# Performance work log

Measured on AMD Instinct MI355X. Metric: run time of the kernel, lower is better.

## Reference

```python
import jax, jax.numpy as jnp
import numpy as np

B, T, C, H, F = 4, 1024, 1024, 16, 4096
D = C // H

def _ln(x, g, b):
    m = x.mean(-1, keepdims=True)
    v = ((x - m) ** 2).mean(-1, keepdims=True)
    return (x - m) * jax.lax.rsqrt(v + 1e-5) * g + b

def setup_inputs() -> dict:
    key = jax.random.key(0)
    ks = jax.random.split(key, 9)
    p = lambda k, shape: jax.random.normal(k, shape, jnp.float32) * 0.02
    return dict(
        x=jax.random.normal(ks[0], (B, T, C), jnp.float32),
        context=jax.random.normal(ks[1], (B, T, C), jnp.float32),
        ln1_g=jnp.ones((C,), jnp.float32), ln1_b=jnp.zeros((C,), jnp.float32),
        qkv_w=p(ks[2], (C, 3 * C)), qkv_b=jnp.zeros((3 * C,), jnp.float32),
        attn_out_w=p(ks[3], (C, C)), attn_out_b=jnp.zeros((C,), jnp.float32),
        lnc_g=jnp.ones((C,), jnp.float32), lnc_b=jnp.zeros((C,), jnp.float32),
        q_w=p(ks[4], (C, C)), q_b=jnp.zeros((C,), jnp.float32),
        kv_w=p(ks[5], (C, 2 * C)), kv_b=jnp.zeros((2 * C,), jnp.float32),
        cross_out_w=p(ks[6], (C, C)), cross_out_b=jnp.zeros((C,), jnp.float32),
        ln2_g=jnp.ones((C,), jnp.float32), ln2_b=jnp.zeros((C,), jnp.float32),
        ffn_w1=p(ks[7], (C, F)), ffn_b1=jnp.zeros((F,), jnp.float32),
        ffn_w2=p(ks[8], (F, C)), ffn_b2=jnp.zeros((C,), jnp.float32),
    )

def reference(x, context, ln1_g, ln1_b, qkv_w, qkv_b, attn_out_w, attn_out_b,
              lnc_g, lnc_b, q_w, q_b, kv_w, kv_b, cross_out_w, cross_out_b,
              ln2_g, ln2_b, ffn_w1, ffn_b1, ffn_w2, ffn_b2):
    scale = 1.0 / np.sqrt(D)
    # --- causal self-attention ---
    h = _ln(x, ln1_g, ln1_b)
    qkv = (h @ qkv_w + qkv_b).reshape(B, T, 3, H, D)
    q, k, v = qkv[:, :, 0], qkv[:, :, 1], qkv[:, :, 2]  # [B,T,H,D]
    s = jnp.einsum('bqhd,bkhd->bhqk', q, k) * scale     # [B,H,T,T]
    causal = jnp.tril(jnp.ones((T, T), bool))
    s = jnp.where(causal, s, -jnp.inf)
    a = jax.nn.softmax(s, axis=-1)
    o = jnp.einsum('bhqk,bkhd->bqhd', a, v).reshape(B, T, C)
    x = x + o @ attn_out_w + attn_out_b
    # --- cross-attention (query=x, context=encoder) ---
    h = _ln(x, lnc_g, lnc_b)
    q = (h @ q_w + q_b).reshape(B, T, H, D)
    kv = (context @ kv_w + kv_b).reshape(B, T, 2, H, D)
    k, v = kv[:, :, 0], kv[:, :, 1]
    s = jnp.einsum('bqhd,bkhd->bhqk', q, k) * scale
    a = jax.nn.softmax(s, axis=-1)
    o = jnp.einsum('bhqk,bkhd->bqhd', a, v).reshape(B, T, C)
    x = x + o @ cross_out_w + cross_out_b
    # --- FFN (exact GELU as in torch default) ---
    h = _ln(x, ln2_g, ln2_b)
    h = jax.nn.gelu(h @ ffn_w1 + ffn_b1, approximate=False)
    return x + h @ ffn_w2 + ffn_b2
```

## Files before the change

### kernel.cpp

```cpp
#include <hip/hip_runtime.h>
#include <hip/hip_bf16.h>

#define BT 4096
#define TT 1024
#define HN 16

typedef __attribute__((ext_vector_type(8))) short bf16x8;
typedef __attribute__((ext_vector_type(4))) float f32x4;
typedef __attribute__((ext_vector_type(16))) float f32x16;

__device__ __forceinline__ unsigned short f2bf(float f) {
    unsigned u = __builtin_bit_cast(unsigned, f);
    unsigned r = (u + 0x7fffu + ((u >> 16) & 1u)) >> 16;
    return (unsigned short)r;
}

__device__ __forceinline__ unsigned pk2bf(float a, float b) {
    return (unsigned)f2bf(a) | ((unsigned)f2bf(b) << 16);
}

__device__ __forceinline__ void g2l16(const void* g, void* l) {
    __builtin_amdgcn_global_load_lds(
        (__attribute__((address_space(1))) void*)(g),
        (__attribute__((address_space(3))) void*)(l), 16, 0, 0);
}

__device__ __forceinline__ float gelu_f(float v) {
    float t = v * (0.7978845608f + 0.0356774081f * v * v);
    float e = __expf(2.f * t);
    float th = 1.f - 2.f / (e + 1.f);
    return 0.5f * v * (1.f + th);
}

struct TransJobs {
    const float* W[7];
    unsigned short* Wt[7];
    int K[7], N[7];
    int start[8];
};

__device__ __forceinline__
void ln_row(const float* __restrict__ xr, const float* __restrict__ g,
            const float* __restrict__ bta, unsigned short* __restrict__ outr,
            float* red)
{
    float4 v = ((const float4*)xr)[threadIdx.x];
    float s = v.x + v.y + v.z + v.w;
    float q = v.x*v.x + v.y*v.y + v.z*v.z + v.w*v.w;
#pragma unroll
    for (int m = 1; m < 64; m <<= 1) {
        s += __shfl_xor(s, m, 64);
        q += __shfl_xor(q, m, 64);
    }
    int wave = threadIdx.x >> 6;
    if ((threadIdx.x & 63) == 0) { red[wave] = s; red[4 + wave] = q; }
    __syncthreads();
    s = red[0] + red[1] + red[2] + red[3];
    q = red[4] + red[5] + red[6] + red[7];
    float mean = s * (1.f / 1024.f);
    float var  = q * (1.f / 1024.f) - mean * mean;
    float rstd = rsqrtf(var + 1e-5f);
    float4 gv = ((const float4*)g)[threadIdx.x];
    float4 bv = ((const float4*)bta)[threadIdx.x];
    uint2 o;
    o.x = pk2bf((v.x - mean) * rstd * gv.x + bv.x, (v.y - mean) * rstd * gv.y + bv.y);
    o.y = pk2bf((v.z - mean) * rstd * gv.z + bv.z, (v.w - mean) * rstd * gv.w + bv.w);
    ((uint2*)outr)[threadIdx.x] = o;
}

__global__ __launch_bounds__(256)
void prep_kernel(TransJobs J, const float* __restrict__ x,
                 const float* __restrict__ g, const float* __restrict__ bta,
                 unsigned short* __restrict__ outx,
                 const float* __restrict__ ctx, unsigned short* __restrict__ outc)
{
    __shared__ float tile[32][33];
    __shared__ float red[8];
    int bid = blockIdx.x;
    const int nT = J.start[7];
    if (bid < nT) {
        int j = 0;
#pragma unroll
        for (int t = 0; t < 7; ++t)
            if (bid >= J.start[t + 1]) j = t + 1;
        int t = bid - J.start[j];
        int K = J.K[j], N = J.N[j];
        int ntx = N >> 5;
        int n0 = (t % ntx) * 32, k0 = (t / ntx) * 32;
        const float* W = J.W[j];
        unsigned short* Wt = J.Wt[j];
        int tx = threadIdx.x & 31, ty = threadIdx.x >> 5;
#pragma unroll
        for (int i = ty; i < 32; i += 8)
            tile[i][tx] = W[(size_t)(k0 + i) * N + n0 + tx];
        __syncthreads();
#pragma unroll
        for (int i = ty; i < 32; i += 8)
            Wt[(size_t)(n0 + i) * K + k0 + tx] = f2bf(tile[tx][i]);
    } else if (bid < nT + BT) {
        int row = bid - nT;
        ln_row(x + (size_t)row * 1024, g, bta, outx + (size_t)row * 1024, red);
    } else {
        size_t i = (size_t)(bid - nT - BT) * 256 + threadIdx.x;
        float4 v = ((const float4*)ctx)[i];
        uint2 o;
        o.x = pk2bf(v.x, v.y);
        o.y = pk2bf(v.z, v.w);
        ((uint2*)outc)[i] = o;
    }
}

__global__ __launch_bounds__(256)
void ln_kernel(const float* __restrict__ x, const float* __restrict__ g,
               const float* __restrict__ bta, unsigned short* __restrict__ out)
{
    __shared__ float red[8];
    int row = blockIdx.x;
    ln_row(x + (size_t)row * 1024, g, bta, out + (size_t)row * 1024, red);
}

__global__ __launch_bounds__(256)
void transpose_v(const unsigned short* __restrict__ v, unsigned short* __restrict__ vt,
                 int stride)
{
    __shared__ unsigned short tile[32][33];
    int d0 = blockIdx.x * 32, t0 = blockIdx.y * 32, bh = blockIdx.z;
    int b = bh >> 4, h = bh & 15;
    int tx = threadIdx.x, ty = threadIdx.y;
#pragma unroll
    for (int i = ty; i < 32; i += 8)
        tile[i][tx] = v[((size_t)b * TT + t0 + i) * stride + h * 64 + d0 + tx];
    __syncthreads();
#pragma unroll
    for (int i = ty; i < 32; i += 8)
        vt[((size_t)bh * 64 + d0 + i) * TT + t0 + tx] = tile[tx][i];
}

template<int MODE>
__device__ __forceinline__
void gemm_core(unsigned short* lA, unsigned short* lB,
               const unsigned short* __restrict__ A,
               const unsigned short* __restrict__ Bt,
               const float* __restrict__ bias,
               const float* __restrict__ res,
               void* __restrict__ outp,
               int N, int K, int m0, int n0, int kbeg, int kend)
{
    const int tid = threadIdx.x;
    const int wave = tid >> 6, lane = tid & 63;
    const int l32 = lane & 31, half = lane >> 5;
    const int sw = l32 & 7;
    const int wN = (wave >> 1) * 64;
    const int wM = (wave & 1) * 64;

    f32x16 acc[2][2];
#pragma unroll
    for (int i = 0; i < 2; ++i)
#pragma unroll
        for (int j = 0; j < 2; ++j)
#pragma unroll
            for (int r = 0; r < 16; ++r) acc[i][j][r] = 0.f;

    for (int k0 = kbeg; k0 < kend; k0 += 64) {
        __syncthreads();
#pragma unroll
        for (int it = 0; it < 4; ++it) {
            int chunk = it * 256 + tid;
            int row = chunk >> 3, slot = chunk & 7;
            int kc = slot ^ (row & 7);
            g2l16(A  + (size_t)(m0 + row) * K + k0 + kc * 8, &lA[chunk * 8]);
            g2l16(Bt + (size_t)(n0 + row) * K + k0 + kc * 8, &lB[chunk * 8]);
        }
        __syncthreads();
#pragma unroll
        for (int ks = 0; ks < 4; ++ks) {
            const int gc = ks * 2 + half;
            const int sl = (gc ^ sw) * 8;
            bf16x8 af[2], bfr[2];
#pragma unroll
            for (int i = 0; i < 2; ++i)
                af[i] = *(const bf16x8*)&lB[(wN + i * 32 + l32) * 64 + sl];
#pragma unroll
            for (int j = 0; j < 2; ++j)
                bfr[j] = *(const bf16x8*)&lA[(wM + j * 32 + l32) * 64 + sl];
#pragma unroll
            for (int i = 0; i < 2; ++i)
#pragma unroll
                for (int j = 0; j < 2; ++j)
                    acc[i][j] = __builtin_amdgcn_mfma_f32_32x32x16_bf16(af[i], bfr[j], acc[i][j], 0, 0, 0);
        }
    }

#pragma unroll
    for (int i = 0; i < 2; ++i) {
#pragma unroll
        for (int g = 0; g < 4; ++g) {
            const int nb = n0 + wN + i * 32 + g * 8 + half * 4;
            float4 bs;
            if (MODE != 3) bs = *(const float4*)&bias[nb];
#pragma unroll
            for (int j = 0; j < 2; ++j) {
                const int m = m0 + wM + j * 32 + l32;
                const size_t idx = (size_t)m * N + nb;
                float v0 = acc[i][j][g * 4 + 0], v1 = acc[i][j][g * 4 + 1];
                float v2 = acc[i][j][g * 4 + 2], v3 = acc[i][j][g * 4 + 3];
                if (MODE != 3) { v0 += bs.x; v1 += bs.y; v2 += bs.z; v3 += bs.w; }
                if (MODE == 1) { v0 = gelu_f(v0); v1 = gelu_f(v1); v2 = gelu_f(v2); v3 = gelu_f(v3); }
                if (MODE == 2) {
                    float4 rr = *(const float4*)&res[idx];
                    float4 o; o.x = v0 + rr.x; o.y = v1 + rr.y; o.z = v2 + rr.z; o.w = v3 + rr.w;
                    *(float4*)((float*)outp + idx) = o;
                } else if (MODE == 3) {
                    float4 o; o.x = v0; o.y = v1; o.z = v2; o.w = v3;
                    *(float4*)((float*)outp + idx) = o;
                } else {
                    uint2 u;
                    u.x = pk2bf(v0, v1);
                    u.y = pk2bf(v2, v3);
                    *(uint2*)((unsigned short*)outp + idx) = u;
                }
            }
        }
    }
}

template<int MODE>
__global__ __launch_bounds__(256)
void gemm_bt(const unsigned short* __restrict__ A,
             const unsigned short* __restrict__ Bt,
             const float* __restrict__ bias,
             const float* __restrict__ res,
             void* __restrict__ outp,
             int M, int N, int K)
{
    __shared__ unsigned short lA[128 * 64];
    __shared__ unsigned short lB[128 * 64];
    gemm_core<MODE>(lA, lB, A, Bt, bias, res, outp, N, K,
                    blockIdx.y * 128, blockIdx.x * 128, 0, K);
}

__global__ __launch_bounds__(256)
void gemm_dual(const unsigned short* __restrict__ A1, const unsigned short* __restrict__ B1,
               const float* __restrict__ b1, unsigned short* __restrict__ o1p, int N1, int nbx1,
               const unsigned short* __restrict__ A2, const unsigned short* __restrict__ B2,
               const float* __restrict__ b2, unsigned short* __restrict__ o2p, int N2,
               int K)
{
    __shared__ unsigned short lA[128 * 64];
    __shared__ unsigned short lB[128 * 64];
    int bx = blockIdx.x;
    if (bx < nbx1)
        gemm_core<0>(lA, lB, A1, B1, b1, nullptr, o1p, N1, K,
                     blockIdx.y * 128, bx * 128, 0, K);
    else
        gemm_core<0>(lA, lB, A2, B2, b2, nullptr, o2p, N2, K,
                     blockIdx.y * 128, (bx - nbx1) * 128, 0, K);
}

__global__ __launch_bounds__(256)
void gemm_splitk(const unsigned short* __restrict__ A,
                 const unsigned short* __restrict__ Bt,
                 float* __restrict__ part,
                 int M, int N, int K, int kslice)
{
    __shared__ unsigned short lA[128 * 64];
    __shared__ unsigned short lB[128 * 64];
    int kz = blockIdx.z;
    gemm_core<3>(lA, lB, A, Bt, nullptr, nullptr,
                 part + (size_t)kz * M * N, N, K,
                 blockIdx.y * 128, blockIdx.x * 128,
                 kz * kslice, (kz + 1) * kslice);
}

__global__ __launch_bounds__(256)
void reduce2(const float* __restrict__ part, const float* __restrict__ bias,
             const float* __restrict__ res, float* __restrict__ out, int MN)
{
    int i = blockIdx.x * 256 + threadIdx.x;
    const float4* p = (const float4*)part;
    int q = MN >> 2;
    float4 a = p[i], b = p[i + q];
    float4 bs = ((const float4*)bias)[i & 255];
    float4 rr = ((const float4*)res)[i];
    float4 o;
    o.x = a.x + b.x + bs.x + rr.x;
    o.y = a.y + b.y + bs.y + rr.y;
    o.z = a.z + b.z + bs.z + rr.z;
    o.w = a.w + b.w + bs.w + rr.w;
    ((float4*)out)[i] = o;
}

__global__ __launch_bounds__(256)
void gemm_small2(const unsigned short* __restrict__ A,
                 const unsigned short* __restrict__ Bt,
                 const float* __restrict__ bias,
                 const float* __restrict__ res,
                 float* __restrict__ outp,
                 int M, int N, int K)
{
    __shared__ unsigned short lA[64 * 64];
    __shared__ unsigned short lB[128 * 64];
    const int tid = threadIdx.x;
    const int wave = tid >> 6, lane = tid & 63;
    const int l32 = lane & 31, half = lane >> 5;
    const int sw = l32 & 7;
    const int m0 = blockIdx.y * 64, n0 = blockIdx.x * 128;
    const int wM = (wave >> 1) * 32;
    const int wN = (wave & 1) * 64;

    f32x16 acc[2];
#pragma unroll
    for (int i = 0; i < 2; ++i)
#pragma unroll
        for (int r = 0; r < 16; ++r) acc[i][r] = 0.f;

    for (int k0 = 0; k0 < K; k0 += 64) {
        __syncthreads();
#pragma unroll
        for (int it = 0; it < 6; ++it) {
            int chunk = it * 256 + tid;
            if (chunk < 512) {
                int row = chunk >> 3, slot = chunk & 7;
                int kc = slot ^ (row & 7);
                g2l16(A + (size_t)(m0 + row) * K + k0 + kc * 8, &lA[chunk * 8]);
            } else {
                int cb = chunk - 512;
                int row = cb >> 3, slot = cb & 7;
                int kc = slot ^ (row & 7);
                g2l16(Bt + (size_t)(n0 + row) * K + k0 + kc * 8, &lB[cb * 8]);
            }
        }
        __syncthreads();
#pragma unroll
        for (int ks = 0; ks < 4; ++ks) {
            const int gc = ks * 2 + half;
            const int sl = (gc ^ sw) * 8;
            bf16x8 bfr = *(const bf16x8*)&lA[(wM + l32) * 64 + sl];
            bf16x8 af[2];
#pragma unroll
            for (int i = 0; i < 2; ++i)
                af[i] = *(const bf16x8*)&lB[(wN + i * 32 + l32) * 64 + sl];
#pragma unroll
            for (int i = 0; i < 2; ++i)
                acc[i] = __builtin_amdgcn_mfma_f32_32x32x16_bf16(af[i], bfr, acc[i], 0, 0, 0);
        }
    }

#pragma unroll
    for (int i = 0; i < 2; ++i) {
#pragma unroll
        for (int g = 0; g < 4; ++g) {
            const int nb = n0 + wN + i * 32 + g * 8 + half * 4;
            float4 bs = *(const float4*)&bias[nb];
            const int m = m0 + wM + l32;
            const size_t idx = (size_t)m * N + nb;
            float4 rr = *(const float4*)&res[idx];
            float4 o;
            o.x = acc[i][g * 4 + 0] + bs.x + rr.x;
            o.y = acc[i][g * 4 + 1] + bs.y + rr.y;
            o.z = acc[i][g * 4 + 2] + bs.z + rr.z;
            o.w = acc[i][g * 4 + 3] + bs.w + rr.w;
            *(float4*)&outp[idx] = o;
        }
    }
}

__global__ __launch_bounds__(256)
void attn_kernel(const unsigned short* __restrict__ qp,
                 const unsigned short* __restrict__ kp,
                 const unsigned short* __restrict__ vt,
                 unsigned short* __restrict__ op,
                 int qstride, int kstride, int causal)
{
    __shared__ unsigned short lK[64 * 72];
    __shared__ unsigned short lV[64 * 72];
    __shared__ unsigned short lP[4][16 * 72];

    const int tid = threadIdx.x;
    const int wave = tid >> 6, lane = tid & 63;
    const int quad = lane >> 4, l16 = lane & 15;
    const int bh = blockIdx.y, b = bh >> 4, h = bh & 15;
    const int qtile = causal ? (gridDim.x - 1 - blockIdx.x) : blockIdx.x;
    const int q0 = qtile * 64;
    const size_t rowbase = (size_t)b * TT;
    const int hoff = h * 64;
    const unsigned short* vbase = vt + (size_t)bh * 64 * TT;

    bf16x8 qf[2];
    {
        int qrow = q0 + wave * 16 + l16;
        const unsigned short* qrp = qp + (rowbase + qrow) * (size_t)qstride + hoff;
        qf[0] = *(const bf16x8*)(qrp + quad * 8);
        qf[1] = *(const bf16x8*)(qrp + 32 + quad * 8);
    }

    f32x4 oacc[4];
#pragma unroll
    for (int jd = 0; jd < 4; ++jd)
#pragma unroll
        for (int r = 0; r < 4; ++r) oacc[jd][r] = 0.f;
    float mrun = -1e30f, lrun = 0.f;

    const int nkt = causal ? (qtile + 1) : (TT / 64);
    for (int kt = 0; kt < nkt; ++kt) {
        __syncthreads();
#pragma unroll
        for (int it = 0; it < 2; ++it) {
            int c = it * 256 + tid;
            int r8 = c >> 3, cc = c & 7;
            *(bf16x8*)&lK[r8 * 72 + cc * 8] =
                *(const bf16x8*)(kp + (rowbase + kt * 64 + r8) * (size_t)kstride + hoff + cc * 8);
            *(bf16x8*)&lV[r8 * 72 + cc * 8] =
                *(const bf16x8*)(vbase + (size_t)r8 * TT + kt * 64 + cc * 8);
        }
        __syncthreads();

        f32x4 s[4];
#pragma unroll
        for (int i = 0; i < 4; ++i)
#pragma unroll
            for (int r = 0; r < 4; ++r) s[i][r] = 0.f;
#pragma unroll
        for (int kk = 0; kk < 2; ++kk) {
            bf16x8 kf[4];
#pragma unroll
            for (int i = 0; i < 4; ++i)
                kf[i] = *(const bf16x8*)&lK[(i * 16 + l16) * 72 + kk * 32 + quad * 8];
#pragma unroll
            for (int i = 0; i < 4; ++i)
                s[i] = __builtin_amdgcn_mfma_f32_16x16x32_bf16(kf[i], qf[kk], s[i], 0, 0, 0);
        }

        const int qg = q0 + wave * 16 + l16;
        const bool domask = (causal != 0) && (kt == qtile);
        float mloc = -1e30f;
#pragma unroll
        for (int i = 0; i < 4; ++i)
#pragma unroll
            for (int r = 0; r < 4; ++r) {
                float v = s[i][r] * 0.125f;
                if (domask) {
                    int kg = kt * 64 + i * 16 + quad * 4 + r;
                    if (kg > qg) v = -1e30f;
                }
                s[i][r] = v;
                mloc = fmaxf(mloc, v);
            }
        mloc = fmaxf(mloc, __shfl_xor(mloc, 16, 64));
        mloc = fmaxf(mloc, __shfl_xor(mloc, 32, 64));
        float mn = fmaxf(mrun, mloc);
        float alpha = __expf(mrun - mn);
        mrun = mn;
        float ls = 0.f;
#pragma unroll
        for (int i = 0; i < 4; ++i)
#pragma unroll
            for (int r = 0; r < 4; ++r) {
                float p = __expf(s[i][r] - mn);
                s[i][r] = p;
                ls += p;
            }
        ls += __shfl_xor(ls, 16, 64);
        ls += __shfl_xor(ls, 32, 64);
        lrun = lrun * alpha + ls;

        float arow[4];
#pragma unroll
        for (int r = 0; r < 4; ++r)
            arow[r] = __shfl(alpha, quad * 4 + r, 64);
#pragma unroll
        for (int jd = 0; jd < 4; ++jd)
#pragma unroll
            for (int r = 0; r < 4; ++r) oacc[jd][r] *= arow[r];

        unsigned short* pw = lP[wave];
#pragma unroll
        for (int i = 0; i < 4; ++i) {
            ushort4 pk;
            pk.x = f2bf(s[i][0]); pk.y = f2bf(s[i][1]);
            pk.z = f2bf(s[i][2]); pk.w = f2bf(s[i][3]);
            *(ushort4*)&pw[l16 * 72 + i * 16 + quad * 4] = pk;
        }

#pragma unroll
        for (int kk = 0; kk < 2; ++kk) {
            bf16x8 pf = *(const bf16x8*)&pw[l16 * 72 + kk * 32 + quad * 8];
            bf16x8 vf[4];
#pragma unroll
            for (int jd = 0; jd < 4; ++jd)
                vf[jd] = *(const bf16x8*)&lV[(jd * 16 + l16) * 72 + kk * 32 + quad * 8];
#pragma unroll
            for (int jd = 0; jd < 4; ++jd)
                oacc[jd] = __builtin_amdgcn_mfma_f32_16x16x32_bf16(pf, vf[jd], oacc[jd], 0, 0, 0);
        }
    }

    float ir[4];
#pragma unroll
    for (int r = 0; r < 4; ++r)
        ir[r] = 1.f / __shfl(lrun, quad * 4 + r, 64);
#pragma unroll
    for (int r = 0; r < 4; ++r) {
        int qg = q0 + wave * 16 + quad * 4 + r;
        unsigned short* orow = op + (rowbase + qg) * (size_t)1024 + hoff;
#pragma unroll
        for (int jd = 0; jd < 4; ++jd)
            orow[jd * 16 + l16] = f2bf(oacc[jd][r] * ir[r]);
    }
}

extern "C" void kernel_launch(void* const* d_in, const int* in_sizes, int n_in,
                              void* d_out, int out_size, void* d_ws, size_t ws_size,
                              hipStream_t stream)
{
    const float* x     = (const float*)d_in[0];
    const float* ctx   = (const float*)d_in[1];
    const float* ln1_g = (const float*)d_in[2];
    const float* ln1_b = (const float*)d_in[3];
    const float* qkv_w = (const float*)d_in[4];
    const float* qkv_b = (const float*)d_in[5];
    const float* aow   = (const float*)d_in[6];
    const float* aob   = (const float*)d_in[7];
    const float* lnc_g = (const float*)d_in[8];
    const float* lnc_b = (const float*)d_in[9];
    const float* q_w   = (const float*)d_in[10];
    const float* q_b   = (const float*)d_in[11];
    const float* kv_w  = (const float*)d_in[12];
    const float* kv_b  = (const float*)d_in[13];
    const float* cow   = (const float*)d_in[14];
    const float* cob   = (const float*)d_in[15];
    const float* ln2_g = (const float*)d_in[16];
    const float* ln2_b = (const float*)d_in[17];
    const float* f1w   = (const float*)d_in[18];
    const float* f1b   = (const float*)d_in[19];
    const float* f2w   = (const float*)d_in[20];
    const float* f2b   = (const float*)d_in[21];

    char* ws = (char*)d_ws;
    size_t off = 0;
    auto alloc = [&](size_t bytes) {
        char* p = ws + off;
        off += (bytes + 255) & ~(size_t)255;
        return p;
    };

    unsigned short* WtQKV = (unsigned short*)alloc((size_t)3072 * 1024 * 2);
    unsigned short* WtAO  = (unsigned short*)alloc((size_t)1024 * 1024 * 2);
    unsigned short* WtQ   = (unsigned short*)alloc((size_t)1024 * 1024 * 2);
    unsigned short* WtKV  = (unsigned short*)alloc((size_t)2048 * 1024 * 2);
    unsigned short* WtCO  = (unsigned short*)alloc((size_t)1024 * 1024 * 2);
    unsigned short* WtF1  = (unsigned short*)alloc((size_t)4096 * 1024 * 2);
    unsigned short* WtF2  = (unsigned short*)alloc((size_t)1024 * 4096 * 2);
    unsigned short* hA    = (unsigned short*)alloc((size_t)BT * 1024 * 2);
    unsigned short* ctxb  = (unsigned short*)alloc((size_t)BT * 1024 * 2);
    unsigned short* qkvb  = (unsigned short*)alloc((size_t)BT * 3072 * 2);
    unsigned short* o1    = (unsigned short*)alloc((size_t)BT * 1024 * 2);
    float*          x1    = (float*)alloc((size_t)BT * 1024 * 4);
    unsigned short* qb    = (unsigned short*)alloc((size_t)BT * 1024 * 2);
    unsigned short* kvb   = (unsigned short*)alloc((size_t)BT * 2048 * 2);
    unsigned short* o2    = (unsigned short*)alloc((size_t)BT * 1024 * 2);
    float*          x2    = (float*)alloc((size_t)BT * 1024 * 4);
    unsigned short* mid   = (unsigned short*)alloc((size_t)BT * 4096 * 2);
    unsigned short* vT1   = (unsigned short*)alloc((size_t)BT * 1024 * 2);
    unsigned short* vT2   = (unsigned short*)alloc((size_t)BT * 1024 * 2);

    float* partials = (float*)qkvb;

    TransJobs J;
    J.W[0]=qkv_w; J.Wt[0]=WtQKV; J.K[0]=1024; J.N[0]=3072;
    J.W[1]=aow;   J.Wt[1]=WtAO;  J.K[1]=1024; J.N[1]=1024;
    J.W[2]=q_w;   J.Wt[2]=WtQ;   J.K[2]=1024; J.N[2]=1024;
    J.W[3]=kv_w;  J.Wt[3]=WtKV;  J.K[3]=1024; J.N[3]=2048;
    J.W[4]=cow;   J.Wt[4]=WtCO;  J.K[4]=1024; J.N[4]=1024;
    J.W[5]=f1w;   J.Wt[5]=WtF1;  J.K[5]=1024; J.N[5]=4096;
    J.W[6]=f2w;   J.Wt[6]=WtF2;  J.K[6]=4096; J.N[6]=1024;
    int acc = 0;
    for (int j = 0; j < 7; ++j) {
        J.start[j] = acc;
        acc += (J.N[j] / 32) * (J.K[j] / 32);
    }
    J.start[7] = acc;

    dim3 tb(32, 8);

    prep_kernel<<<acc + 2 * BT, 256, 0, stream>>>(J, x, ln1_g, ln1_b, hA, ctx, ctxb);

    gemm_bt<0><<<dim3(3072/128, BT/128), 256, 0, stream>>>(hA, WtQKV, qkv_b, nullptr, qkvb, BT, 3072, 1024);
    transpose_v<<<dim3(2, TT/32, 64), tb, 0, stream>>>(qkvb + 2048, vT1, 3072);
    attn_kernel<<<dim3(TT/64, 64), 256, 0, stream>>>(qkvb, qkvb + 1024, vT1, o1, 3072, 3072, 1);
    gemm_small2<<<dim3(1024/128, BT/64), 256, 0, stream>>>(o1, WtAO, aob, x, x1, BT, 1024, 1024);

    ln_kernel<<<BT, 256, 0, stream>>>(x1, lnc_g, lnc_b, hA);
    gemm_dual<<<dim3(1024/128 + 2048/128, BT/128), 256, 0, stream>>>(
        hA, WtQ, q_b, qb, 1024, 1024/128,
        ctxb, WtKV, kv_b, kvb, 2048, 1024);
    transpose_v<<<dim3(2, TT/32, 64), tb, 0, stream>>>(kvb + 1024, vT2, 2048);
    attn_kernel<<<dim3(TT/64, 64), 256, 0, stream>>>(qb, kvb, vT2, o2, 1024, 2048, 0);
    gemm_small2<<<dim3(1024/128, BT/64), 256, 0, stream>>>(o2, WtCO, cob, x1, x2, BT, 1024, 1024);

    ln_kernel<<<BT, 256, 0, stream>>>(x2, ln2_g, ln2_b, hA);
    gemm_bt<1><<<dim3(4096/128, BT/128), 256, 0, stream>>>(hA, WtF1, f1b, nullptr, mid, BT, 4096, 1024);
    gemm_splitk<<<dim3(1024/128, BT/128, 2), 256, 0, stream>>>(mid, WtF2, partials, BT, 1024, 4096, 2048);
    reduce2<<<BT * 1024 / 4 / 256, 256, 0, stream>>>(partials, f2b, x2, (float*)d_out, BT * 1024);
}
```

Measured before the change: 533.2 us.

## Double-buffer LDS tiles in GEMM kernels to overlap loads with MFMA

The GEMM core and the small-M GEMM now use two LDS buffers per operand. The next K-tile is prefetched with global_load_lds while the current tile is consumed by MFMA, and only one barrier is needed per iteration. This is meant to hide global-to-LDS latency that the old load-sync-compute loop exposed. In exchange, LDS use per block doubles, which may lower occupancy. Correctness depends on the barrier waiting for the outstanding async LDS loads.

```diff
diff --git a/kernel.cpp b/kernel.cpp
--- a/kernel.cpp
+++ b/kernel.cpp
@@ -136,9 +136,26 @@
         vt[((size_t)bh * 64 + d0 + i) * TT + t0 + tx] = tile[tx][i];
 }
 
+
+__device__ __forceinline__
+void stage128(const unsigned short* __restrict__ A,
+              const unsigned short* __restrict__ Bt,
+              unsigned short* lA, unsigned short* lB,
+              int m0, int n0, int K, int k0, int tid)
+{
+#pragma unroll
+    for (int it = 0; it < 4; ++it) {
+        int chunk = it * 256 + tid;
+        int row = chunk >> 3, slot = chunk & 7;
+        int kc = slot ^ (row & 7);
+        g2l16(A  + (size_t)(m0 + row) * K + k0 + kc * 8, &lA[chunk * 8]);
+        g2l16(Bt + (size_t)(n0 + row) * K + k0 + kc * 8, &lB[chunk * 8]);
+    }
+}
+
 template<int MODE>
 __device__ __forceinline__
-void gemm_core(unsigned short* lA, unsigned short* lB,
+void gemm_core(unsigned short (*lA)[128 * 64], unsigned short (*lB)[128 * 64],
                const unsigned short* __restrict__ A,
                const unsigned short* __restrict__ Bt,
                const float* __restrict__ bias,
@@ -161,17 +178,16 @@
 #pragma unroll
             for (int r = 0; r < 16; ++r) acc[i][j][r] = 0.f;
 
-    for (int k0 = kbeg; k0 < kend; k0 += 64) {
+    const int nIter = (kend - kbeg) >> 6;
+    stage128(A, Bt, lA[0], lB[0], m0, n0, K, kbeg, tid);
+
+    for (int it = 0; it < nIter; ++it) {
         __syncthreads();
-#pragma unroll
-        for (int it = 0; it < 4; ++it) {
-            int chunk = it * 256 + tid;
-            int row = chunk >> 3, slot = chunk & 7;
-            int kc = slot ^ (row & 7);
-            g2l16(A  + (size_t)(m0 + row) * K + k0 + kc * 8, &lA[chunk * 8]);
-            g2l16(Bt + (size_t)(n0 + row) * K + k0 + kc * 8, &lB[chunk * 8]);
-        }
-        __syncthreads();
+        const int cur = it & 1, nxt = cur ^ 1;
+        if (it + 1 < nIter)
+            stage128(A, Bt, lA[nxt], lB[nxt], m0, n0, K, kbeg + (it + 1) * 64, tid);
+        const unsigned short* cA = lA[cur];
+        const unsigned short* cB = lB[cur];
 #pragma unroll
         for (int ks = 0; ks < 4; ++ks) {
             const int gc = ks * 2 + half;
@@ -179,10 +195,10 @@
             bf16x8 af[2], bfr[2];
 #pragma unroll
             for (int i = 0; i < 2; ++i)
-                af[i] = *(const bf16x8*)&lB[(wN + i * 32 + l32) * 64 + sl];
+                af[i] = *(const bf16x8*)&cB[(wN + i * 32 + l32) * 64 + sl];
 #pragma unroll
             for (int j = 0; j < 2; ++j)
-                bfr[j] = *(const bf16x8*)&lA[(wM + j * 32 + l32) * 64 + sl];
+                bfr[j] = *(const bf16x8*)&cA[(wM + j * 32 + l32) * 64 + sl];
 #pragma unroll
             for (int i = 0; i < 2; ++i)
 #pragma unroll
@@ -233,8 +249,8 @@
              void* __restrict__ outp,
              int M, int N, int K)
 {
-    __shared__ unsigned short lA[128 * 64];
-    __shared__ unsigned short lB[128 * 64];
+    __shared__ unsigned short lA[2][128 * 64];
+    __shared__ unsigned short lB[2][128 * 64];
     gemm_core<MODE>(lA, lB, A, Bt, bias, res, outp, N, K,
                     blockIdx.y * 128, blockIdx.x * 128, 0, K);
 }
@@ -246,8 +262,8 @@
                const float* __restrict__ b2, unsigned short* __restrict__ o2p, int N2,
                int K)
 {
-    __shared__ unsigned short lA[128 * 64];
-    __shared__ unsigned short lB[128 * 64];
+    __shared__ unsigned short lA[2][128 * 64];
+    __shared__ unsigned short lB[2][128 * 64];
     int bx = blockIdx.x;
     if (bx < nbx1)
         gemm_core<0>(lA, lB, A1, B1, b1, nullptr, o1p, N1, K,
@@ -263,8 +279,8 @@
                  float* __restrict__ part,
                  int M, int N, int K, int kslice)
 {
-    __shared__ unsigned short lA[128 * 64];
-    __shared__ unsigned short lB[128 * 64];
+    __shared__ unsigned short lA[2][128 * 64];
+    __shared__ unsigned short lB[2][128 * 64];
     int kz = blockIdx.z;
     gemm_core<3>(lA, lB, A, Bt, nullptr, nullptr,
                  part + (size_t)kz * M * N, N, K,
@@ -298,8 +314,8 @@
                  float* __restrict__ outp,
                  int M, int N, int K)
 {
-    __shared__ unsigned short lA[64 * 64];
-    __shared__ unsigned short lB[128 * 64];
+    __shared__ unsigned short lA[2][64 * 64];
+    __shared__ unsigned short lB[2][128 * 64];
     const int tid = threadIdx.x;
     const int wave = tid >> 6, lane = tid & 63;
     const int l32 = lane & 31, half = lane >> 5;
@@ -314,32 +330,40 @@
 #pragma unroll
         for (int r = 0; r < 16; ++r) acc[i][r] = 0.f;
 
-    for (int k0 = 0; k0 < K; k0 += 64) {
-        __syncthreads();
+    auto stage = [&](int buf, int k0) {
 #pragma unroll
         for (int it = 0; it < 6; ++it) {
             int chunk = it * 256 + tid;
             if (chunk < 512) {
                 int row = chunk >> 3, slot = chunk & 7;
                 int kc = slot ^ (row & 7);
-                g2l16(A + (size_t)(m0 + row) * K + k0 + kc * 8, &lA[chunk * 8]);
+                g2l16(A + (size_t)(m0 + row) * K + k0 + kc * 8, &lA[buf][chunk * 8]);
             } else {
                 int cb = chunk - 512;
                 int row = cb >> 3, slot = cb & 7;
                 int kc = slot ^ (row & 7);
-                g2l16(Bt + (size_t)(n0 + row) * K + k0 + kc * 8, &lB[cb * 8]);
+                g2l16(Bt + (size_t)(n0 + row) * K + k0 + kc * 8, &lB[buf][cb * 8]);
             }
         }
+    };
+
+    const int nIter = K >> 6;
+    stage(0, 0);
+    for (int it = 0; it < nIter; ++it) {
         __syncthreads();
+        const int cur = it & 1, nxt = cur ^ 1;
+        if (it + 1 < nIter) stage(nxt, (it + 1) * 64);
+        const unsigned short* cA = lA[cur];
+        const unsigned short* cB = lB[cur];
 #pragma unroll
         for (int ks = 0; ks < 4; ++ks) {
             const int gc = ks * 2 + half;
             const int sl = (gc ^ sw) * 8;
-            bf16x8 bfr = *(const bf16x8*)&lA[(wM + l32) * 64 + sl];
+            bf16x8 bfr = *(const bf16x8*)&cA[(wM + l32) * 64 + sl];
             bf16x8 af[2];
 #pragma unroll
             for (int i = 0; i < 2; ++i)
-                af[i] = *(const bf16x8*)&lB[(wN + i * 32 + l32) * 64 + sl];
+                af[i] = *(const bf16x8*)&cB[(wN + i * 32 + l32) * 64 + sl];
 #pragma unroll
             for (int i = 0; i < 2; ++i)
                 acc[i] = __builtin_amdgcn_mfma_f32_32x32x16_bf16(af[i], bfr, acc[i], 0, 0, 0);
```

New measurement: 556.9 us. 4.4% more time.
